# Kernel optimization log

Measured on AMD Instinct MI355X. Metric: run time of the kernel, lower is better.

Reference implementation:

```python
import jax, jax.numpy as jnp
import numpy as np

N_NODES = 100000
N_EDGES = 1600000
D_FEAT = 128
HIDDEN = 64


def setup_inputs() -> dict:
    key = jax.random.key(0)
    k1, k2, k3, k4, k5 = jax.random.split(key, 5)
    x = jax.random.normal(k1, (N_NODES, D_FEAT), dtype=jnp.float32)
    edge_index = jax.random.randint(k2, (2, N_EDGES), 0, N_NODES, dtype=jnp.int32)
    edge_weight = jax.random.uniform(k3, (N_EDGES,), dtype=jnp.float32)
    W1 = jax.random.normal(k4, (D_FEAT, HIDDEN), dtype=jnp.float32) / np.sqrt(D_FEAT)
    b1 = jnp.zeros((HIDDEN,), dtype=jnp.float32)
    W2 = jax.random.normal(k5, (HIDDEN, 1), dtype=jnp.float32) / np.sqrt(HIDDEN)
    b2 = jnp.zeros((1,), dtype=jnp.float32)
    return {"x": x, "edge_index": edge_index, "edge_weight": edge_weight,
            "W1": W1, "b1": b1, "W2": W2, "b2": b2}


def reference(x, edge_index, edge_weight, W1, b1, W2, b2):
    N = x.shape[0]
    # PyG GCNConv default: add self-loops with weight 1.0
    loops = jnp.arange(N, dtype=edge_index.dtype)
    row = jnp.concatenate([edge_index[0], loops])  # source nodes
    col = jnp.concatenate([edge_index[1], loops])  # target nodes
    ew = jnp.concatenate([edge_weight, jnp.ones((N,), dtype=edge_weight.dtype)])
    # symmetric degree normalization: norm_e = d^{-1/2}[row] * w_e * d^{-1/2}[col]
    deg = jax.ops.segment_sum(ew, col, num_segments=N)
    dinv = jnp.where(deg > 0, jax.lax.rsqrt(deg), 0.0)
    norm = dinv[row] * ew * dinv[col]  # [E+N]

    def gcn_layer(h, W, b):
        h = h @ W                          # [N, out] transform first (PyG order)
        msg = h[row] * norm[:, None]       # gather + scale, [E+N, out]
        agg = jax.ops.segment_sum(msg, col, num_segments=N)  # scatter-add
        return agg + b

    h = jax.nn.relu(gcn_layer(x, W1, b1))
    # dropout(p=0.5) is identity in eval mode
    return gcn_layer(h, W2, b2)  # [N, 1]
```

## Files before the change

kernel.cpp:

```cpp
#include <hip/hip_runtime.h>
#include <stdint.h>

typedef float f4 __attribute__((ext_vector_type(4)));
typedef float f32x4 __attribute__((ext_vector_type(4)));
typedef _Float16 hq4 __attribute__((ext_vector_type(4)));
typedef _Float16 half8 __attribute__((ext_vector_type(8)));

#define DF 128
#define HID 64
#define EPB 4096
#define CAP 5120

__global__ __launch_bounds__(512) void kFused(const int* __restrict__ row,
                                              const int* __restrict__ col,
                                              const float* __restrict__ ew,
                                              int* __restrict__ cur,
                                              int2* __restrict__ tmp,
                                              const float* __restrict__ x,
                                              const float* __restrict__ W1,
                                              float* __restrict__ g,
                                              int E, int nblk, int nstrip, int N) {
    __shared__ __align__(16) char smem[55360];
    int t = threadIdx.x;

    if ((int)blockIdx.x < nblk) {
        int*  hist  = (int*)smem;
        int*  pref  = hist + 512;
        int*  lbase = pref + 512;
        int*  wsum  = lbase + 512;
        int2* sv    = (int2*)(smem + 6208);
        int*  sa    = (int*)(smem + 6208 + 32768);
        int b = blockIdx.x;
        hist[t] = 0;
        __syncthreads();
        int s = b * EPB, e = min(E, s + EPB);
        int cnt = e - s;
        int  mybin[8], myrank[8];
        int2 myv[8];
#pragma unroll
        for (int k = 0; k < 8; ++k) {
            int i = s + t + k * 512;
            mybin[k] = -1;
            if (i < e) {
                int c = col[i];
                int bin = c >> 8;
                myv[k].x = row[i] | ((c & 255) << 24);
                myv[k].y = __float_as_int(ew[i]);
                mybin[k] = bin;
                myrank[k] = atomicAdd(&hist[bin], 1);
            }
        }
        __syncthreads();
        int val = hist[t];
        lbase[t] = val ? atomicAdd(&cur[t], val) + t * CAP : 0;
        int lane = t & 63, wid = t >> 6;
        int inc = val;
#pragma unroll
        for (int d = 1; d < 64; d <<= 1) {
            int y = __shfl_up(inc, d);
            if (lane >= d) inc += y;
        }
        if (lane == 63) wsum[wid] = inc;
        __syncthreads();
        if (t == 0) {
            int r = 0;
#pragma unroll
            for (int i = 0; i < 8; ++i) { int xx = wsum[i]; wsum[i] = r; r += xx; }
        }
        __syncthreads();
        pref[t] = inc - val + wsum[wid];
        __syncthreads();
#pragma unroll
        for (int k = 0; k < 8; ++k) {
            if (mybin[k] >= 0) {
                int pos = pref[mybin[k]] + myrank[k];
                sv[pos] = myv[k];
                sa[pos] = lbase[mybin[k]] + myrank[k];
            }
        }
        __syncthreads();
        for (int i = t; i < cnt; i += 512) tmp[sa[i]] = sv[i];
    } else {
        _Float16* W1f = (_Float16*)smem;
        for (int i = t; i < 8192; i += 512) {
            int j     = i & 7;
            int lane  = (i >> 3) & 63;
            int ntile = (i >> 9) & 3;
            int kstep = i >> 11;
            int k = kstep * 32 + (lane >> 4) * 8 + j;
            int n = ntile * 16 + (lane & 15);
            W1f[i] = (_Float16)W1[k * 64 + n];
        }
        __syncthreads();
        int wave = ((int)blockIdx.x - nblk) * 8 + (t >> 6);
        if (wave >= nstrip) return;
        int node0 = wave << 4;
        int l = t & 63;
        int quad = l >> 4;
        int m = l & 15;
        int r = node0 + m;
        if (r >= N) r = N - 1;

        const half8* bfrag = (const half8*)W1f;
        f32x4 acc[4];
#pragma unroll
        for (int nt = 0; nt < 4; ++nt) acc[nt] = (f32x4)(0.f);
#pragma unroll
        for (int kstep = 0; kstep < 4; ++kstep) {
            const f4* xr = (const f4*)(x + (size_t)r * DF + kstep * 32 + quad * 8);
            f4 a0 = xr[0], a1 = xr[1];
            half8 af;
            af[0] = (_Float16)a0.x; af[1] = (_Float16)a0.y;
            af[2] = (_Float16)a0.z; af[3] = (_Float16)a0.w;
            af[4] = (_Float16)a1.x; af[5] = (_Float16)a1.y;
            af[6] = (_Float16)a1.z; af[7] = (_Float16)a1.w;
#pragma unroll
            for (int nt = 0; nt < 4; ++nt) {
                half8 bf = bfrag[(kstep * 4 + nt) * 64 + l];
                acc[nt] = __builtin_amdgcn_mfma_f32_16x16x32_f16(af, bf, acc[nt], 0, 0, 0);
            }
        }
        int nodeb = node0 + quad * 4;
#pragma unroll
        for (int nt = 0; nt < 4; ++nt) {
#pragma unroll
            for (int reg = 0; reg < 4; ++reg) {
                int node = nodeb + reg;
                if (node < N)
                    g[(size_t)node * 64 + (unsigned)(nt * 16 + m)] = acc[nt][reg];
            }
        }
    }
}

__global__ __launch_bounds__(512) void kB(const int2* __restrict__ tmp,
                                          const int* __restrict__ cur,
                                          const float* __restrict__ g,
                                          int2* __restrict__ edata,
                                          int2* __restrict__ offse,
                                          float* __restrict__ dinv,
                                          _Float16* __restrict__ h,
                                          int N) {
    __shared__ int   hist[256];
    __shared__ float degl[256];
    __shared__ int   fill[256];
    __shared__ float dl[256];
    __shared__ int   wsum[8];
    __shared__ int2  se[CAP];
    int bin = blockIdx.x, t = threadIdx.x;
    int s = bin * CAP;
    int cnt = min(cur[bin], CAP);

    if (t < 256) { hist[t] = 0; degl[t] = 0.f; }
    __syncthreads();
    for (int i = t; i < cnt; i += 512) {
        int2 pr = tmp[s + i];
        se[i] = pr;
        int lo = ((unsigned)pr.x) >> 24;
        atomicAdd(&hist[lo], 1);
        atomicAdd(&degl[lo], __int_as_float(pr.y));
    }
    __syncthreads();
    int val = (t < 256) ? hist[t] : 0;
    int lane = t & 63, wid = t >> 6;
    int inc = val;
#pragma unroll
    for (int d = 1; d < 64; d <<= 1) {
        int y = __shfl_up(inc, d);
        if (lane >= d) inc += y;
    }
    if (lane == 63) wsum[wid] = inc;
    __syncthreads();
    if (t == 0) {
        int r = 0;
#pragma unroll
        for (int i = 0; i < 8; ++i) { int x = wsum[i]; wsum[i] = r; r += x; }
    }
    __syncthreads();
    int pfx = inc - val + wsum[wid];
    if (t < 256) {
        fill[t] = pfx;
        int c = bin * 256 + t;
        float di = 0.f;
        if (c < N) {
            int2 oe;
            oe.x = s + pfx;
            oe.y = s + pfx + val;
            offse[c] = oe;
            di = rsqrtf(1.0f + degl[t]);
            dinv[c] = di;
        }
        dl[t] = di;
    }
    __syncthreads();
    for (int i = t; i < cnt; i += 512) {
        int2 pr = se[i];
        int lo = ((unsigned)pr.x) >> 24;
        int pos = atomicAdd(&fill[lo], 1);
        int2 o;
        o.x = pr.x & 0x00FFFFFF;
        o.y = pr.y;
        edata[s + pos] = o;
    }
    int vbase = bin << 8;
    for (int i = t; i < 256 * 64; i += 512) {
        int c = i >> 6;
        int v = vbase + c;
        if (v < N)
            h[(size_t)v * 64 + (i & 63)] =
                (_Float16)(dl[c] * g[(size_t)v * 64 + (i & 63)]);
    }
}

__global__ __launch_bounds__(256) void k_agg_h2(const int2* __restrict__ offse,
                                                const int2* __restrict__ edata,
                                                const float* __restrict__ dinv,
                                                const _Float16* __restrict__ h,
                                                const float* __restrict__ b1,
                                                const float* __restrict__ W2,
                                                float* __restrict__ h2p, int N) {
    __shared__ int2 stage[4][68];
    int wv = threadIdx.x >> 6;
    int l  = threadIdx.x & 63;
    int g  = l >> 4;
    unsigned fq = (unsigned)(l & 15);
    int sbase = g * 17;
    int vv = blockIdx.x * 16 + wv * 4 + g;
    bool ok = vv < N;
    int v = ok ? vv : N - 1;
    const hq4* hp = (const hq4*)h;

    float di = dinv[v];
    int2 oe = offse[v];

    hq4 sv4 = hp[((unsigned)v << 4) | fq];
    float a0 = (float)sv4.x, a1 = (float)sv4.y;
    float a2 = (float)sv4.z, a3 = (float)sv4.w;

    int deg = oe.y - oe.x;
    for (int base = 0; base < deg; base += 16) {
        int idx = oe.x + base + (int)fq;
        int2 pr;
        pr.x = 0; pr.y = 0;
        if (idx < oe.y) pr = edata[idx];
        stage[wv][sbase + (int)fq] = pr;
#pragma unroll
        for (int k = 0; k < 16; ++k) {
            int2 em = stage[wv][sbase + k];
            float w = __int_as_float(em.y);
            hq4 hv = hp[((unsigned)em.x << 4) | fq];
            a0 += w * (float)hv.x;
            a1 += w * (float)hv.y;
            a2 += w * (float)hv.z;
            a3 += w * (float)hv.w;
        }
    }

    a0 = di * a0; a1 = di * a1; a2 = di * a2; a3 = di * a3;
    f4 bb = ((const f4*)b1)[fq];
    f4 ww = ((const f4*)W2)[fq];
    float s = fmaxf(a0 + bb.x, 0.f) * ww.x
            + fmaxf(a1 + bb.y, 0.f) * ww.y
            + fmaxf(a2 + bb.z, 0.f) * ww.z
            + fmaxf(a3 + bb.w, 0.f) * ww.w;
    s += __shfl_down(s, 8);
    s += __shfl_down(s, 4);
    s += __shfl_down(s, 2);
    s += __shfl_down(s, 1);
    if (fq == 0 && ok) h2p[vv] = di * s;
}

__global__ __launch_bounds__(256) void k_out(const int2* __restrict__ offse,
                                             const int2* __restrict__ edata,
                                             const float* __restrict__ dinv,
                                             const float* __restrict__ h2p,
                                             const float* __restrict__ b2,
                                             float* __restrict__ out, int N) {
    int t = blockIdx.x * 256 + threadIdx.x;
    int v = t >> 4;
    if (v >= N) return;
    int c = t & 15;
    int2 oe = offse[v];
    float s = 0.f;
    for (int i = oe.x + c; i < oe.y; i += 16) {
        int2 pr = edata[i];
        s += __int_as_float(pr.y) * h2p[(unsigned)pr.x];
    }
    s += __shfl_down(s, 8);
    s += __shfl_down(s, 4);
    s += __shfl_down(s, 2);
    s += __shfl_down(s, 1);
    if (c == 0) {
        float di = dinv[v];
        out[v] = b2[0] + di * (h2p[v] + s);
    }
}

extern "C" void kernel_launch(void* const* d_in, const int* in_sizes, int n_in,
                              void* d_out, int out_size, void* d_ws, size_t ws_size,
                              hipStream_t stream) {
    const float* x  = (const float*)d_in[0];
    const int*   ei = (const int*)d_in[1];
    const float* ew = (const float*)d_in[2];
    const float* W1 = (const float*)d_in[3];
    const float* b1 = (const float*)d_in[4];
    const float* W2 = (const float*)d_in[5];
    const float* b2 = (const float*)d_in[6];
    float* out = (float*)d_out;

    const int N = in_sizes[0] / DF;
    const int E = in_sizes[2];
    const int* row = ei;
    const int* col = ei + E;

    const int nbin = (N + 255) / 256;
    const int nblk = (E + EPB - 1) / EPB;

    size_t    gsz   = (size_t)nbin * CAP;
    int2*     edata = (int2*)d_ws;
    int2*     tmp   = edata + gsz;
    float*    g     = (float*)(tmp + gsz);
    _Float16* h     = (_Float16*)(g + (size_t)N * 64);
    float*    dinv  = (float*)(h + (size_t)N * 64);
    float*    h2p   = dinv + N;
    int2*     offse = (int2*)(h2p + N);
    int*      cur   = (int*)(offse + N);

    const int B = 256;
    int nstrip = (N + 15) / 16;
    int gemmBlocks = (nstrip + 7) / 8;
    int gAgg = (N + 15) / 16;
    int gN16 = (N * 16 + B - 1) / B;

    hipMemsetAsync(cur, 0, nbin * sizeof(int), stream);
    kFused<<<nblk + gemmBlocks, 512, 0, stream>>>(row, col, ew, cur, tmp,
                                                  x, W1, g, E, nblk, nstrip, N);
    kB<<<nbin, 512, 0, stream>>>(tmp, cur, g, edata, offse, dinv, h, N);
    k_agg_h2<<<gAgg, B, 0, stream>>>(offse, edata, dinv, h, b1, W2, h2p, N);
    k_out<<<gN16, B, 0, stream>>>(offse, edata, dinv, h2p, b2, out, N);
}
```

Before: 204.3 us.

## Compute degrees with global atomics in bucketing pass and fuse normalization into GEMM

Weighted in-degrees are now accumulated with global float atomics during the first bucketing pass, so the GEMM can apply the d^{-1/2} scaling directly and write the half-precision h. The GEMM moves out of the first kernel and shares a launch with the per-bin CSR build, and W1 is pre-swizzled to global memory by one extra block. This removes the fp32 g intermediate (a write plus a re-read) and the dinv array, since later kernels recompute rsqrt from degw. In exchange it adds 1.6M global atomics on random addresses and makes degree sums order-nondeterministic.

```diff
diff --git a/kernel.cpp b/kernel.cpp
--- a/kernel.cpp
+++ b/kernel.cpp
@@ -11,77 +11,17 @@
 #define EPB 4096
 #define CAP 5120
 
-__global__ __launch_bounds__(512) void kFused(const int* __restrict__ row,
-                                              const int* __restrict__ col,
-                                              const float* __restrict__ ew,
-                                              int* __restrict__ cur,
-                                              int2* __restrict__ tmp,
-                                              const float* __restrict__ x,
-                                              const float* __restrict__ W1,
-                                              float* __restrict__ g,
-                                              int E, int nblk, int nstrip, int N) {
-    __shared__ __align__(16) char smem[55360];
-    int t = threadIdx.x;
-
-    if ((int)blockIdx.x < nblk) {
-        int*  hist  = (int*)smem;
-        int*  pref  = hist + 512;
-        int*  lbase = pref + 512;
-        int*  wsum  = lbase + 512;
-        int2* sv    = (int2*)(smem + 6208);
-        int*  sa    = (int*)(smem + 6208 + 32768);
-        int b = blockIdx.x;
-        hist[t] = 0;
-        __syncthreads();
-        int s = b * EPB, e = min(E, s + EPB);
-        int cnt = e - s;
-        int  mybin[8], myrank[8];
-        int2 myv[8];
-#pragma unroll
-        for (int k = 0; k < 8; ++k) {
-            int i = s + t + k * 512;
-            mybin[k] = -1;
-            if (i < e) {
-                int c = col[i];
-                int bin = c >> 8;
-                myv[k].x = row[i] | ((c & 255) << 24);
-                myv[k].y = __float_as_int(ew[i]);
-                mybin[k] = bin;
-                myrank[k] = atomicAdd(&hist[bin], 1);
-            }
-        }
-        __syncthreads();
-        int val = hist[t];
-        lbase[t] = val ? atomicAdd(&cur[t], val) + t * CAP : 0;
-        int lane = t & 63, wid = t >> 6;
-        int inc = val;
-#pragma unroll
-        for (int d = 1; d < 64; d <<= 1) {
-            int y = __shfl_up(inc, d);
-            if (lane >= d) inc += y;
-        }
-        if (lane == 63) wsum[wid] = inc;
-        __syncthreads();
-        if (t == 0) {
-            int r = 0;
-#pragma unroll
-            for (int i = 0; i < 8; ++i) { int xx = wsum[i]; wsum[i] = r; r += xx; }
-        }
-        __syncthreads();
-        pref[t] = inc - val + wsum[wid];
-        __syncthreads();
-#pragma unroll
-        for (int k = 0; k < 8; ++k) {
-            if (mybin[k] >= 0) {
-                int pos = pref[mybin[k]] + myrank[k];
-                sv[pos] = myv[k];
-                sa[pos] = lbase[mybin[k]] + myrank[k];
-            }
-        }
-        __syncthreads();
-        for (int i = t; i < cnt; i += 512) tmp[sa[i]] = sv[i];
-    } else {
-        _Float16* W1f = (_Float16*)smem;
+__global__ __launch_bounds__(512) void kA3(const int* __restrict__ row,
+                                           const int* __restrict__ col,
+                                           const float* __restrict__ ew,
+                                           int* __restrict__ cur,
+                                           float* __restrict__ degw,
+                                           int2* __restrict__ tmp,
+                                           const float* __restrict__ W1,
+                                           _Float16* __restrict__ W1f,
+                                           int E, int nblk) {
+    int b = blockIdx.x, t = threadIdx.x;
+    if (b == nblk) {
         for (int i = t; i < 8192; i += 512) {
             int j     = i & 7;
             int lane  = (i >> 3) & 63;
@@ -91,8 +31,133 @@
             int n = ntile * 16 + (lane & 15);
             W1f[i] = (_Float16)W1[k * 64 + n];
         }
-        __syncthreads();
-        int wave = ((int)blockIdx.x - nblk) * 8 + (t >> 6);
+        return;
+    }
+    __shared__ int hist[512];
+    __shared__ int pref[512];
+    __shared__ int lbase[512];
+    __shared__ int wsum[8];
+    __shared__ int2 sv[EPB];
+    __shared__ int  sa[EPB];
+    hist[t] = 0;
+    __syncthreads();
+    int s = b * EPB, e = min(E, s + EPB);
+    int cnt = e - s;
+    int  mybin[8], myrank[8];
+    int2 myv[8];
+#pragma unroll
+    for (int k = 0; k < 8; ++k) {
+        int i = s + t + k * 512;
+        mybin[k] = -1;
+        if (i < e) {
+            int c = col[i];
+            float w = ew[i];
+            int bin = c >> 8;
+            myv[k].x = row[i] | ((c & 255) << 24);
+            myv[k].y = __float_as_int(w);
+            mybin[k] = bin;
+            myrank[k] = atomicAdd(&hist[bin], 1);
+            unsafeAtomicAdd(&degw[c], w);
+        }
+    }
+    __syncthreads();
+    int val = hist[t];
+    lbase[t] = val ? atomicAdd(&cur[t], val) + t * CAP : 0;
+    int lane = t & 63, wid = t >> 6;
+    int inc = val;
+#pragma unroll
+    for (int d = 1; d < 64; d <<= 1) {
+        int y = __shfl_up(inc, d);
+        if (lane >= d) inc += y;
+    }
+    if (lane == 63) wsum[wid] = inc;
+    __syncthreads();
+    if (t == 0) {
+        int r = 0;
+#pragma unroll
+        for (int i = 0; i < 8; ++i) { int xx = wsum[i]; wsum[i] = r; r += xx; }
+    }
+    __syncthreads();
+    pref[t] = inc - val + wsum[wid];
+    __syncthreads();
+#pragma unroll
+    for (int k = 0; k < 8; ++k) {
+        if (mybin[k] >= 0) {
+            int pos = pref[mybin[k]] + myrank[k];
+            sv[pos] = myv[k];
+            sa[pos] = lbase[mybin[k]] + myrank[k];
+        }
+    }
+    __syncthreads();
+    for (int i = t; i < cnt; i += 512) tmp[sa[i]] = sv[i];
+}
+
+__global__ __launch_bounds__(512) void kMid(const int2* __restrict__ tmp,
+                                            const int* __restrict__ cur,
+                                            int2* __restrict__ edata,
+                                            int2* __restrict__ offse,
+                                            const float* __restrict__ x,
+                                            const _Float16* __restrict__ W1f,
+                                            const float* __restrict__ degw,
+                                            _Float16* __restrict__ h,
+                                            int nbin, int nstrip, int N) {
+    __shared__ int   hist[256];
+    __shared__ int   fill[256];
+    __shared__ int   wsum[8];
+    __shared__ int2  se[CAP];
+    int t = threadIdx.x;
+
+    if ((int)blockIdx.x < nbin) {
+        int bin = blockIdx.x;
+        int s = bin * CAP;
+        int cnt = min(cur[bin], CAP);
+        if (t < 256) hist[t] = 0;
+        __syncthreads();
+        for (int i = t; i < cnt; i += 512) {
+            int2 pr = tmp[s + i];
+            se[i] = pr;
+            atomicAdd(&hist[((unsigned)pr.x) >> 24], 1);
+        }
+        __syncthreads();
+        int val = (t < 256) ? hist[t] : 0;
+        int lane = t & 63, wid = t >> 6;
+        int inc = val;
+#pragma unroll
+        for (int d = 1; d < 64; d <<= 1) {
+            int y = __shfl_up(inc, d);
+            if (lane >= d) inc += y;
+        }
+        if (lane == 63) wsum[wid] = inc;
+        __syncthreads();
+        if (t == 0) {
+            int r = 0;
+#pragma unroll
+            for (int i = 0; i < 8; ++i) { int xx = wsum[i]; wsum[i] = r; r += xx; }
+        }
+        __syncthreads();
+        int pfx = inc - val + wsum[wid];
+        if (t < 256) {
+            fill[t] = pfx;
+            int c = bin * 256 + t;
+            if (c < N) {
+                int2 oe;
+                oe.x = s + pfx;
+                oe.y = s + pfx + val;
+                offse[c] = oe;
+            }
+        }
+        __syncthreads();
+        for (int i = t; i < cnt; i += 512) {
+            int2 pr = se[i];
+            int lo = ((unsigned)pr.x) >> 24;
+            int pos = atomicAdd(&fill[lo], 1);
+            int2 o;
+            o.x = pr.x & 0x00FFFFFF;
+            o.y = pr.y;
+            edata[s + pos] = o;
+        }
+    } else {
+        int wave = ((int)blockIdx.x - nbin) * 8 + (t >> 6);
         if (wave >= nstrip) return;
         int node0 = wave << 4;
         int l = t & 63;
@@ -120,101 +185,27 @@
                 acc[nt] = __builtin_amdgcn_mfma_f32_16x16x32_f16(af, bf, acc[nt], 0, 0, 0);
             }
         }
+        float dv[4];
         int nodeb = node0 + quad * 4;
+#pragma unroll
+        for (int reg = 0; reg < 4; ++reg)
+            dv[reg] = (nodeb + reg < N) ? rsqrtf(1.f + degw[nodeb + reg]) : 0.f;
 #pragma unroll
         for (int nt = 0; nt < 4; ++nt) {
 #pragma unroll
             for (int reg = 0; reg < 4; ++reg) {
                 int node = nodeb + reg;
                 if (node < N)
-                    g[(size_t)node * 64 + (unsigned)(nt * 16 + m)] = acc[nt][reg];
+                    h[(unsigned)node * 64u + (unsigned)(nt * 16 + m)] =
+                        (_Float16)(dv[reg] * acc[nt][reg]);
             }
         }
-    }
-}
-
-__global__ __launch_bounds__(512) void kB(const int2* __restrict__ tmp,
-                                          const int* __restrict__ cur,
-                                          const float* __restrict__ g,
-                                          int2* __restrict__ edata,
-                                          int2* __restrict__ offse,
-                                          float* __restrict__ dinv,
-                                          _Float16* __restrict__ h,
-                                          int N) {
-    __shared__ int   hist[256];
-    __shared__ float degl[256];
-    __shared__ int   fill[256];
-    __shared__ float dl[256];
-    __shared__ int   wsum[8];
-    __shared__ int2  se[CAP];
-    int bin = blockIdx.x, t = threadIdx.x;
-    int s = bin * CAP;
-    int cnt = min(cur[bin], CAP);
-
-    if (t < 256) { hist[t] = 0; degl[t] = 0.f; }
-    __syncthreads();
-    for (int i = t; i < cnt; i += 512) {
-        int2 pr = tmp[s + i];
-        se[i] = pr;
-        int lo = ((unsigned)pr.x) >> 24;
-        atomicAdd(&hist[lo], 1);
-        atomicAdd(&degl[lo], __int_as_float(pr.y));
-    }
-    __syncthreads();
-    int val = (t < 256) ? hist[t] : 0;
-    int lane = t & 63, wid = t >> 6;
-    int inc = val;
-#pragma unroll
-    for (int d = 1; d < 64; d <<= 1) {
-        int y = __shfl_up(inc, d);
-        if (lane >= d) inc += y;
-    }
-    if (lane == 63) wsum[wid] = inc;
-    __syncthreads();
-    if (t == 0) {
-        int r = 0;
-#pragma unroll
-        for (int i = 0; i < 8; ++i) { int x = wsum[i]; wsum[i] = r; r += x; }
-    }
-    __syncthreads();
-    int pfx = inc - val + wsum[wid];
-    if (t < 256) {
-        fill[t] = pfx;
-        int c = bin * 256 + t;
-        float di = 0.f;
-        if (c < N) {
-            int2 oe;
-            oe.x = s + pfx;
-            oe.y = s + pfx + val;
-            offse[c] = oe;
-            di = rsqrtf(1.0f + degl[t]);
-            dinv[c] = di;
-        }
-        dl[t] = di;
-    }
-    __syncthreads();
-    for (int i = t; i < cnt; i += 512) {
-        int2 pr = se[i];
-        int lo = ((unsigned)pr.x) >> 24;
-        int pos = atomicAdd(&fill[lo], 1);
-        int2 o;
-        o.x = pr.x & 0x00FFFFFF;
-        o.y = pr.y;
-        edata[s + pos] = o;
-    }
-    int vbase = bin << 8;
-    for (int i = t; i < 256 * 64; i += 512) {
-        int c = i >> 6;
-        int v = vbase + c;
-        if (v < N)
-            h[(size_t)v * 64 + (i & 63)] =
-                (_Float16)(dl[c] * g[(size_t)v * 64 + (i & 63)]);
     }
 }
 
 __global__ __launch_bounds__(256) void k_agg_h2(const int2* __restrict__ offse,
                                                 const int2* __restrict__ edata,
-                                                const float* __restrict__ dinv,
+                                                const float* __restrict__ degw,
                                                 const _Float16* __restrict__ h,
                                                 const float* __restrict__ b1,
                                                 const float* __restrict__ W2,
@@ -230,7 +221,7 @@
     int v = ok ? vv : N - 1;
     const hq4* hp = (const hq4*)h;
 
-    float di = dinv[v];
+    float di = rsqrtf(1.f + degw[v]);
     int2 oe = offse[v];
 
     hq4 sv4 = hp[((unsigned)v << 4) | fq];
@@ -272,7 +263,7 @@
 
 __global__ __launch_bounds__(256) void k_out(const int2* __restrict__ offse,
                                              const int2* __restrict__ edata,
-                                             const float* __restrict__ dinv,
+                                             const float* __restrict__ degw,
                                              const float* __restrict__ h2p,
                                              const float* __restrict__ b2,
                                              float* __restrict__ out, int N) {
@@ -291,7 +282,7 @@
     s += __shfl_down(s, 2);
     s += __shfl_down(s, 1);
     if (c == 0) {
-        float di = dinv[v];
+        float di = rsqrtf(1.f + degw[v]);
         out[v] = b2[0] + di * (h2p[v] + s);
     }
 }
@@ -319,12 +310,13 @@
     size_t    gsz   = (size_t)nbin * CAP;
     int2*     edata = (int2*)d_ws;
     int2*     tmp   = edata + gsz;
-    float*    g     = (float*)(tmp + gsz);
-    _Float16* h     = (_Float16*)(g + (size_t)N * 64);
-    float*    dinv  = (float*)(h + (size_t)N * 64);
-    float*    h2p   = dinv + N;
+    _Float16* h     = (_Float16*)(tmp + gsz);
+    int       nbinPad = (nbin + 3) & ~3;
+    int*      cur   = (int*)(h + (size_t)N * 64);
+    float*    degw  = (float*)(cur + nbinPad);
+    float*    h2p   = degw + N;
     int2*     offse = (int2*)(h2p + N);
-    int*      cur   = (int*)(offse + N);
+    _Float16* W1f   = (_Float16*)(offse + N);
 
     const int B = 256;
     int nstrip = (N + 15) / 16;
@@ -332,10 +324,12 @@
     int gAgg = (N + 15) / 16;
     int gN16 = (N * 16 + B - 1) / B;
 
-    hipMemsetAsync(cur, 0, nbin * sizeof(int), stream);
-    kFused<<<nblk + gemmBlocks, 512, 0, stream>>>(row, col, ew, cur, tmp,
-                                                  x, W1, g, E, nblk, nstrip, N);
-    kB<<<nbin, 512, 0, stream>>>(tmp, cur, g, edata, offse, dinv, h, N);
-    k_agg_h2<<<gAgg, B, 0, stream>>>(offse, edata, dinv, h, b1, W2, h2p, N);
-    k_out<<<gN16, B, 0, stream>>>(offse, edata, dinv, h2p, b2, out, N);
-}
+    hipMemsetAsync(cur, 0, (size_t)(nbinPad + N) * sizeof(int), stream);
+    kA3<<<nblk + 1, 512, 0, stream>>>(row, col, ew, cur, degw, tmp, W1, W1f,
+                                      E, nblk);
+    kMid<<<nbin + gemmBlocks, 512, 0, stream>>>(tmp, cur, edata, offse,
+                                                x, W1f, degw, h,
+                                                nbin, nstrip, N);
+    k_agg_h2<<<gAgg, B, 0, stream>>>(offse, edata, degw, h, b1, W2, h2p, N);
+    k_out<<<gN16, B, 0, stream>>>(offse, edata, degw, h2p, b2, out, N);
+}
```

Result: slower. 254.9 us (+24.7%).
